# Performance work log

Measured on AMD Instinct MI355X. Metric: run time of the kernel, lower is better.

## Reference

```python
import jax, jax.numpy as jnp
import numpy as np

EPS = 1e-8
HIDDEN = 200


def _dsmall(n, d):
    # torch: d = d*(d>eps) + eps*(d<=eps); n/d
    return n / jnp.where(d > EPS, d, EPS)


def _mp_match(v1, v2, w):
    # v1: (B,S,H); v2: (B,S,H) or (B,H); w: (L,H) -> (B,S,L)
    wt = w.T[None, None]                      # (1,1,H,L)
    a = v1[..., None] * wt                    # (B,S,H,L)
    if v2.ndim == 2:
        v2 = jnp.broadcast_to(v2[:, None, :], v1.shape)
    b = v2[..., None] * wt                    # (B,S,H,L)
    dot = jnp.sum(a * b, axis=2)
    na = jnp.linalg.norm(a, axis=2)
    nb = jnp.linalg.norm(b, axis=2)
    return dot / jnp.maximum(na * nb, EPS)    # cosine_similarity over H


def _mp_pairwise(v1, v2, w):
    # v1: (B,S1,H); v2: (B,S2,H); w: (L,H) -> (B,S1,S2,L)
    a = v1[:, None] * w[None, :, None]        # (B,L,S1,H)
    b = v2[:, None] * w[None, :, None]        # (B,L,S2,H)
    na = jnp.linalg.norm(a, axis=3, keepdims=True)   # (B,L,S1,1)
    nb = jnp.linalg.norm(b, axis=3, keepdims=True)   # (B,L,S2,1)
    n = jnp.einsum('blph,blqh->blpq', a, b)
    d = na * jnp.swapaxes(nb, 2, 3)
    return jnp.transpose(_dsmall(n, d), (0, 2, 3, 1))


def _attention(v1, v2):
    # cosine-similarity matrix (B,S1,S2)
    n1 = jnp.linalg.norm(v1, axis=2, keepdims=True)           # (B,S1,1)
    n2 = jnp.linalg.norm(v2, axis=2, keepdims=True)           # (B,S2,1)
    a = jnp.einsum('bph,bqh->bpq', v1, v2)
    return _dsmall(a, n1 * jnp.swapaxes(n2, 1, 2))


def _matching(con_p, con_h, w1, w2, w3, w4, w5, w6, w7, w8):
    p_fw, p_bw = con_p[..., :HIDDEN], con_p[..., HIDDEN:]
    h_fw, h_bw = con_h[..., :HIDDEN], con_h[..., HIDDEN:]

    # 1) full matching
    mv_p_full_fw = _mp_match(p_fw, h_fw[:, -1, :], w1)
    mv_p_full_bw = _mp_match(p_bw, h_bw[:, 0, :], w2)
    mv_h_full_fw = _mp_match(h_fw, p_fw[:, -1, :], w1)
    mv_h_full_bw = _mp_match(h_bw, p_bw[:, 0, :], w2)

    # 2) maxpooling matching
    mv_max_fw = _mp_pairwise(p_fw, h_fw, w3)  # (B,S1,S2,L)
    mv_max_bw = _mp_pairwise(p_bw, h_bw, w4)
    mv_p_max_fw = jnp.max(mv_max_fw, axis=2)
    mv_p_max_bw = jnp.max(mv_max_bw, axis=2)
    mv_h_max_fw = jnp.max(mv_max_fw, axis=1)
    mv_h_max_bw = jnp.max(mv_max_bw, axis=1)

    # 3) attentive matching (mean)
    att_fw = _attention(p_fw, h_fw)           # (B,S1,S2)
    att_bw = _attention(p_bw, h_bw)

    # sum of att_h over dim 2 is a matmul (same math, no (B,S1,S2,H) tensor)
    att_h_sum_fw = jnp.einsum('bpq,bqh->bph', att_fw, h_fw)
    att_h_sum_bw = jnp.einsum('bpq,bqh->bph', att_bw, h_bw)
    att_p_sum_fw = jnp.einsum('bpq,bph->bqh', att_fw, p_fw)
    att_p_sum_bw = jnp.einsum('bpq,bph->bqh', att_bw, p_bw)

    att_mean_h_fw = _dsmall(att_h_sum_fw, jnp.sum(att_fw, axis=2, keepdims=True))
    att_mean_h_bw = _dsmall(att_h_sum_bw, jnp.sum(att_bw, axis=2, keepdims=True))
    att_mean_p_fw = _dsmall(att_p_sum_fw, jnp.swapaxes(jnp.sum(att_fw, axis=1, keepdims=True), 1, 2))
    att_mean_p_bw = _dsmall(att_p_sum_bw, jnp.swapaxes(jnp.sum(att_bw, axis=1, keepdims=True), 1, 2))

    mv_p_att_mean_fw = _mp_match(p_fw, att_mean_h_fw, w5)
    mv_p_att_mean_bw = _mp_match(p_bw, att_mean_h_bw, w6)
    mv_h_att_mean_fw = _mp_match(h_fw, att_mean_p_fw, w5)
    mv_h_att_mean_bw = _mp_match(h_bw, att_mean_p_bw, w6)

    # 4) max-attentive matching (needs full (B,S1,S2,H) broadcast for the max)
    att_h_fw = h_fw[:, None, :, :] * att_fw[:, :, :, None]   # (B,S1,S2,H)
    att_h_bw = h_bw[:, None, :, :] * att_bw[:, :, :, None]
    att_p_fw = p_fw[:, :, None, :] * att_fw[:, :, :, None]
    att_p_bw = p_bw[:, :, None, :] * att_bw[:, :, :, None]

    att_max_h_fw = jnp.max(att_h_fw, axis=2)                 # (B,S1,H)
    att_max_h_bw = jnp.max(att_h_bw, axis=2)
    att_max_p_fw = jnp.max(att_p_fw, axis=1)                 # (B,S2,H)
    att_max_p_bw = jnp.max(att_p_bw, axis=1)

    mv_p_att_max_fw = _mp_match(p_fw, att_max_h_fw, w7)
    mv_p_att_max_bw = _mp_match(p_bw, att_max_h_bw, w8)
    mv_h_att_max_fw = _mp_match(h_fw, att_max_p_fw, w7)
    mv_h_att_max_bw = _mp_match(h_bw, att_max_p_bw, w8)

    mv_p = jnp.concatenate([mv_p_full_fw, mv_p_max_fw, mv_p_att_mean_fw, mv_p_att_max_fw,
                            mv_p_full_bw, mv_p_max_bw, mv_p_att_mean_bw, mv_p_att_max_bw], axis=2)
    mv_h = jnp.concatenate([mv_h_full_fw, mv_h_max_fw, mv_h_att_mean_fw, mv_h_att_max_fw,
                            mv_h_full_bw, mv_h_max_bw, mv_h_att_mean_bw, mv_h_att_max_bw], axis=2)
    # dropout is identity in inference mode
    return mv_p, mv_h


def setup_inputs() -> dict:
    key = jax.random.key(0)
    ks = jax.random.split(key, 10)
    B, S, H, L = 32, 64, HIDDEN, 20
    w_std = np.sqrt(2.0 / H)  # kaiming_normal fan_in
    inp = {
        'con_p': jax.random.normal(ks[0], (B, S, 2 * H), dtype=jnp.float32),
        'con_h': jax.random.normal(ks[1], (B, S, 2 * H), dtype=jnp.float32),
    }
    for i in range(8):
        inp[f'mp_w{i+1}'] = jax.random.normal(ks[2 + i], (L, H), dtype=jnp.float32) * w_std
    return inp


def reference(con_p, con_h, mp_w1, mp_w2, mp_w3, mp_w4, mp_w5, mp_w6, mp_w7, mp_w8):
    return _matching(con_p, con_h, mp_w1, mp_w2, mp_w3, mp_w4, mp_w5, mp_w6, mp_w7, mp_w8)
```

## Files before the change

kernel.cpp:

```cpp
#include <hip/hip_runtime.h>
#include <hip/hip_bf16.h>
#include <math.h>

#define EPS 1e-8f
#define BB 32
#define SS 64
#define HH 200
#define LL 20
#define KST 232
#define S16ST 72
#define BHST 72
#define MLST 208

typedef short bf16x8 __attribute__((ext_vector_type(8)));
typedef float f32x4 __attribute__((ext_vector_type(4)));
typedef _Float16 f16x8v __attribute__((ext_vector_type(8)));
typedef _Float16 f16x2 __attribute__((ext_vector_type(2)));

__global__ __launch_bounds__(512, 4) void fused_all_kernel(
        const float* __restrict__ conp, const float* __restrict__ conh,
        const float* __restrict__ w1, const float* __restrict__ w2,
        const float* __restrict__ w3, const float* __restrict__ w4,
        const float* __restrict__ w5, const float* __restrict__ w6,
        const float* __restrict__ w7, const float* __restrict__ w8,
        float* __restrict__ out) {
    __shared__ __align__(16) float smem[19104];
    int t = threadIdx.x;

    int wg = ((blockIdx.x & 7) * 96) + (blockIdx.x >> 3);
    int grp = wg / 3;
    int rem = wg % 3;

    if (rem < 2) {
        _Float16* AT16 = (_Float16*)smem;
        _Float16* BT16 = (_Float16*)(smem + 1856);
        _Float16* BHh  = (_Float16*)(smem + 9280);
        _Float16* S16h = (_Float16*)(smem + 16768);
        float* nrmA  = smem + 17344;
        float* nrmB  = smem + 17360;
        _Float16* meanLh = (_Float16*)(smem + 17440);
        _Float16* PB = (_Float16*)smem;
        _Float16* WB = (_Float16*)(smem + 5568);

        int blk = grp * 2 + rem;
        int qh = blk & 3;
        int sdb = blk >> 2;
        int b = sdb & 31, sd = sdb >> 5;
        int dir = sd & 1, side = sd >> 1;
        const float* selfb = side ? conh : conp;
        const float* oppb  = side ? conp : conh;
        int fidx = dir ? 0 : (SS - 1);
        const float* fvr = oppb + (b * SS + fidx) * (2 * HH) + dir * HH;

        int arow = t / 25, ack = t % 25;

        float xr[8], yv0[8];
        if (t < 400) {
            const float* xp = selfb + (b * SS + qh * 16 + arow) * (2 * HH) + dir * HH + ack * 8;
            *(float4*)&xr[0] = *(const float4*)xp; *(float4*)&xr[4] = *(const float4*)(xp + 4);
            *(float4*)&yv0[0] = *(const float4*)(fvr + ack * 8);
            *(float4*)&yv0[4] = *(const float4*)(fvr + ack * 8 + 4);
            f16x8v r8;
#pragma unroll
            for (int i = 0; i < 8; ++i) r8[i] = (_Float16)xr[i];
            *(f16x8v*)&AT16[arow * KST + ack * 8] = r8;
        }
        {
            f16x8v z8 = (f16x8v)(_Float16)0.f;
            if (t < 312) {
                if (t < 48) { int row = t / 3, ckp = 25 + t % 3;
                    *(f16x8v*)&AT16[row * KST + ckp * 8] = z8;
                } else if (t < 240) { int e2 = t - 48; int row = e2 / 3, ckp = 25 + e2 % 3;
                    *(f16x8v*)&BT16[row * KST + ckp * 8] = z8;
                } else { int e2 = t - 240; int row = 200 + e2 / 9, c8 = (e2 % 9) * 8;
                    *(f16x8v*)&BHh[row * BHST + c8] = z8;
                }
            }
        }
        for (int e = t; e < 1600; e += 512) {
            int rw = e / 25, ck = e % 25, k = ck * 8;
            const float* xp = oppb + (b * SS + rw) * (2 * HH) + dir * HH + k;
            float xv[8];
            *(float4*)&xv[0] = *(const float4*)xp; *(float4*)&xv[4] = *(const float4*)(xp + 4);
            f16x8v r8;
#pragma unroll
            for (int i = 0; i < 8; ++i) r8[i] = (_Float16)xv[i];
            *(f16x8v*)&BT16[rw * KST + k] = r8;
        }
        __syncthreads();

        int wv_ = __builtin_amdgcn_readfirstlane(t >> 6);
        int lane = t & 63;
        int q = lane >> 4, c = lane & 15;

        f32x4 accS = (f32x4){0.f, 0.f, 0.f, 0.f};
        if (wv_ < 4) {
            int ct = wv_;
            for (int ks = 0; ks < 7; ++ks) {
                int kb = ks * 32 + q * 8;
                f16x8v af  = *(const f16x8v*)&AT16[c * KST + kb];
                f16x8v bf_ = *(const f16x8v*)&BT16[(ct * 16 + c) * KST + kb];
                accS = __builtin_amdgcn_mfma_f32_16x16x32_f16(af, bf_, accS, 0, 0, 0);
            }
        } else {
            int dt = wv_ - 4;
            f32x4 accB = (f32x4){0.f, 0.f, 0.f, 0.f};
            for (int ks = 0; ks < 7; ++ks) {
                int kb = ks * 32 + q * 8;
                f16x8v bf_ = *(const f16x8v*)&BT16[(dt * 16 + c) * KST + kb];
                accB = __builtin_amdgcn_mfma_f32_16x16x32_f16(bf_, bf_, accB, 0, 0, 0);
            }
            if ((c >> 2) == q) nrmB[dt * 16 + c] = accB[c & 3];
            if (dt == 0) {
                f32x4 accA = (f32x4){0.f, 0.f, 0.f, 0.f};
                for (int ks = 0; ks < 7; ++ks) {
                    int kb = ks * 32 + q * 8;
                    f16x8v af = *(const f16x8v*)&AT16[c * KST + kb];
                    accA = __builtin_amdgcn_mfma_f32_16x16x32_f16(af, af, accA, 0, 0, 0);
                }
                if ((c >> 2) == q) nrmA[c] = accA[c & 3];
            } else {
                for (int ch = dt - 1; ch < 25; ch += 3) {
                    f16x8v v = *(const f16x8v*)&BT16[lane * KST + ch * 8];
#pragma unroll
                    for (int i = 0; i < 8; ++i) BHh[(ch * 8 + i) * BHST + lane] = v[i];
                }
            }
        }
        __syncthreads();

        if (wv_ < 4) {
            int col = wv_ * 16 + c;
            float no = sqrtf(nrmB[col]);
#pragma unroll
            for (int r = 0; r < 4; ++r) {
                int row = q * 4 + r;
                float ns = sqrtf(nrmA[row]);
                S16h[row * S16ST + col] = (_Float16)(accS[r] / fmaxf(ns * no, EPS));
            }
        }
        __syncthreads();

        float wf0[8], wf1[8], wf2[8];
        if (t < 500) {
            int wl = t / 25, wck = t % 25;
            const float* wp0 = (dir ? w2 : w1) + wl * HH + wck * 8;
            const float* wp1 = (dir ? w6 : w5) + wl * HH + wck * 8;
            const float* wp2 = (dir ? w8 : w7) + wl * HH + wck * 8;
            *(float4*)&wf0[0] = *(const float4*)wp0; *(float4*)&wf0[4] = *(const float4*)(wp0 + 4);
            *(float4*)&wf1[0] = *(const float4*)wp1; *(float4*)&wf1[4] = *(const float4*)(wp1 + 4);
            *(float4*)&wf2[0] = *(const float4*)wp2; *(float4*)&wf2[4] = *(const float4*)(wp2 + 4);
        }

        f16x2 mx0, mx1, mx2, mx3;
        {
            f16x2 ninf = {(_Float16)(-INFINITY), (_Float16)(-INFINITY)};
            mx0 = ninf; mx1 = ninf; mx2 = ninf; mx3 = ninf;
        }
        if (wv_ == 7) {
            for (int nt = 0; nt < 13; ++nt) {
                f32x4 macc = (f32x4){0.f, 0.f, 0.f, 0.f};
#pragma unroll
                for (int k2 = 0; k2 < 2; ++k2) {
                    int kb = k2 * 32 + q * 8;
                    f16x8v sa = *(const f16x8v*)&S16h[c * S16ST + kb];
                    f16x8v bh = *(const f16x8v*)&BHh[(nt * 16 + c) * BHST + kb];
                    macc = __builtin_amdgcn_mfma_f32_16x16x32_f16(sa, bh, macc, 0, 0, 0);
                }
                int h = nt * 16 + c;
                if (h < 200) {
#pragma unroll
                    for (int r = 0; r < 4; ++r)
                        meanLh[(q * 4 + r) * MLST + h] = (_Float16)(macc[r] * 0.125f);
                }
            }
        } else if (t < 400) {
            const _Float16* srow = &S16h[arow * S16ST];
            const _Float16* bcol = &BT16[ack * 8];
            for (int kg = 0; kg < 8; ++kg) {
                f16x8v sr = *(const f16x8v*)&srow[kg * 8];
#pragma unroll
                for (int kk = 0; kk < 8; ++kk) {
                    _Float16 sh = sr[kk];
                    f16x2 sv = {sh, sh};
                    f16x8v bv = *(const f16x8v*)&bcol[(kg * 8 + kk) * KST];
                    f16x2 p0 = sv * __builtin_shufflevector(bv, bv, 0, 1);
                    f16x2 p1 = sv * __builtin_shufflevector(bv, bv, 2, 3);
                    f16x2 p2 = sv * __builtin_shufflevector(bv, bv, 4, 5);
                    f16x2 p3 = sv * __builtin_shufflevector(bv, bv, 6, 7);
                    mx0 = __builtin_elementwise_max(mx0, p0);
                    mx1 = __builtin_elementwise_max(mx1, p1);
                    mx2 = __builtin_elementwise_max(mx2, p2);
                    mx3 = __builtin_elementwise_max(mx3, p3);
                }
            }
        }
        __syncthreads();

#pragma unroll
        for (int m = 0; m < 3; ++m) {
            if (t < 400) {
                float yv[8];
                if (m == 0) {
#pragma unroll
                    for (int i = 0; i < 8; ++i) yv[i] = yv0[i];
                } else if (m == 1) {
                    f16x8v yl = *(const f16x8v*)&meanLh[arow * MLST + ack * 8];
#pragma unroll
                    for (int i = 0; i < 8; ++i) yv[i] = (float)yl[i];
                } else {
                    yv[0] = (float)mx0[0]; yv[1] = (float)mx0[1];
                    yv[2] = (float)mx1[0]; yv[3] = (float)mx1[1];
                    yv[4] = (float)mx2[0]; yv[5] = (float)mx2[1];
                    yv[6] = (float)mx3[0]; yv[7] = (float)mx3[1];
                }
                f16x8v r1, r2;
#pragma unroll
                for (int i = 0; i < 8; ++i) {
                    r1[i] = (_Float16)(xr[i] * yv[i]);
                    r2[i] = (_Float16)(yv[i] * yv[i]);
                }
                if (m == 0) {
                    f16x8v r0;
#pragma unroll
                    for (int i = 0; i < 8; ++i) r0[i] = (_Float16)(xr[i] * xr[i]);
                    *(f16x8v*)&PB[(0 * 16 + arow) * KST + ack * 8] = r0;
                }
                *(f16x8v*)&PB[(1 * 16 + arow) * KST + ack * 8] = r1;
                *(f16x8v*)&PB[(2 * 16 + arow) * KST + ack * 8] = r2;
            }
            if (t < 500) {
                int wl = t / 25, wck = t % 25;
                f16x8v wr;
                if (m == 0) {
#pragma unroll
                    for (int i = 0; i < 8; ++i) wr[i] = (_Float16)(wf0[i] * wf0[i]);
                } else if (m == 1) {
#pragma unroll
                    for (int i = 0; i < 8; ++i) wr[i] = (_Float16)(wf1[i] * wf1[i]);
                } else {
#pragma unroll
                    for (int i = 0; i < 8; ++i) wr[i] = (_Float16)(wf2[i] * wf2[i]);
                }
                *(f16x8v*)&WB[wl * KST + wck * 8] = wr;
            }
            if (m == 0) {
                f16x8v z8 = (f16x8v)(_Float16)0.f;
                for (int e = t; e < 540; e += 512) {
                    if (e < 144) { int row = e / 3, ckp = 25 + e % 3;
                        *(f16x8v*)&PB[row * KST + ckp * 8] = z8;
                    } else if (e < 480) { int e2 = e - 144; int row = 20 + e2 / 28, ckp = e2 % 28;
                        *(f16x8v*)&WB[row * KST + ckp * 8] = z8;
                    } else { int e2 = e - 480; int row = e2 / 3, ckp = 25 + e2 % 3;
                        *(f16x8v*)&WB[row * KST + ckp * 8] = z8;
                    }
                }
            }
            __syncthreads();

            if (wv_ < 2) {
                int ntile = wv_;
                f32x4 accA = (f32x4){0.f, 0.f, 0.f, 0.f};
                f32x4 accD = (f32x4){0.f, 0.f, 0.f, 0.f};
                f32x4 accB = (f32x4){0.f, 0.f, 0.f, 0.f};
                for (int ks = 0; ks < 7; ++ks) {
                    int kb = ks * 32 + q * 8;
                    f16x8v bfw = *(const f16x8v*)&WB[(ntile * 16 + c) * KST + kb];
                    f16x8v a0 = *(const f16x8v*)&PB[(0 * 16 + c) * KST + kb];
                    f16x8v a1 = *(const f16x8v*)&PB[(1 * 16 + c) * KST + kb];
                    f16x8v a2 = *(const f16x8v*)&PB[(2 * 16 + c) * KST + kb];
                    accA = __builtin_amdgcn_mfma_f32_16x16x32_f16(a0, bfw, accA, 0, 0, 0);
                    accD = __builtin_amdgcn_mfma_f32_16x16x32_f16(a1, bfw, accD, 0, 0, 0);
                    accB = __builtin_amdgcn_mfma_f32_16x16x32_f16(a2, bfw, accB, 0, 0, 0);
                }
                int l_ = ntile * 16 + c;
                if (l_ < LL) {
                    int chunk = (m == 0) ? 0 : (m == 1) ? 40 : 60;
#pragma unroll
                    for (int r = 0; r < 4; ++r) {
                        int s = qh * 16 + q * 4 + r;
                        float cosv = accD[r] / fmaxf(sqrtf(accA[r] * accB[r]), EPS);
                        out[side * (BB * SS * 160) + (b * SS + s) * 160 + dir * 80 + chunk + l_] = cosv;
                    }
                }
            }
            if (m < 2) __syncthreads();
        }
    } else {
        _Float16* ATr = (_Float16*)smem;
        _Float16* BTr = (_Float16*)(smem + 7424);
        _Float16* w2L = (_Float16*)(smem + 14848);
        float* nA5  = smem + 15432;
        float* nB5  = smem + 15752;
        float* cmL5 = smem + 16072;

        int cblk = grp;
        int lg = cblk & 3;
        int db = cblk >> 2;
        int b = db & 31, dir = db >> 5;
        int l0 = lg * 5;
        const float* wsrc = dir ? w4 : w3;
        const float* Ag = conp + dir * HH;
        const float* Bg = conh + dir * HH;

        for (int e = t; e < 3200; e += 512) {
            int half = (e >= 1600) ? 1 : 0;
            int e2 = e - half * 1600;
            int rw = e2 / 25, ck = e2 % 25, k = ck * 8;
            const float* xp = (half ? Bg : Ag) + (b * SS + rw) * (2 * HH) + k;
            float xv[8];
            *(float4*)&xv[0] = *(const float4*)xp; *(float4*)&xv[4] = *(const float4*)(xp + 4);
            f16x8v r8;
#pragma unroll
            for (int i = 0; i < 8; ++i) r8[i] = (_Float16)xv[i];
            _Float16* dst = half ? BTr : ATr;
            *(f16x8v*)&dst[rw * KST + k] = r8;
        }
        {
            f16x8v z8 = (f16x8v)(_Float16)0.f;
            if (t < 384) {
                int half = (t >= 192) ? 1 : 0;
                int e2 = t - half * 192;
                int row = e2 / 3, ckp = 25 + e2 % 3;
                _Float16* dst = half ? BTr : ATr;
                *(f16x8v*)&dst[row * KST + ckp * 8] = z8;
            } else if (t < 399) {
                int e2 = t - 384;
                int wl = e2 / 3, ckp = 25 + e2 % 3;
                *(f16x8v*)&w2L[wl * KST + ckp * 8] = z8;
            }
            if (t < 125) {
                int wl = t / 25, wck = t % 25;
                const float* wp = wsrc + (l0 + wl) * HH + wck * 8;
                float wvv[8];
                *(float4*)&wvv[0] = *(const float4*)wp; *(float4*)&wvv[4] = *(const float4*)(wp + 4);
                f16x8v r8;
#pragma unroll
                for (int i = 0; i < 8; ++i) r8[i] = (_Float16)(wvv[i] * wvv[i]);
                *(f16x8v*)&w2L[wl * KST + wck * 8] = r8;
            }
        }
        __syncthreads();

        int wv_ = __builtin_amdgcn_readfirstlane(t >> 6);
        int lane = t & 63;
        int q = lane >> 4, c = lane & 15;
        int m0 = (wv_ & 3) * 16;

        f32x4 z4 = (f32x4){0.f, 0.f, 0.f, 0.f};
        f32x4 acc0[4] = {z4, z4, z4, z4};
        f32x4 acc1[4] = {z4, z4, z4, z4};
        f32x4 acc2[4] = {z4, z4, z4, z4};

        if (wv_ < 4) {
            for (int ks = 0; ks < 7; ++ks) {
                int kb = ks * 32 + q * 8;
                f16x8v ar  = *(const f16x8v*)&ATr[(m0 + c) * KST + kb];
                f16x8v ww0 = *(const f16x8v*)&w2L[0 * KST + kb];
                f16x8v ww1 = *(const f16x8v*)&w2L[1 * KST + kb];
                f16x8v ww2 = *(const f16x8v*)&w2L[2 * KST + kb];
                f16x8v af0 = ar * ww0, af1 = ar * ww1, af2 = ar * ww2;
#pragma unroll
                for (int ct = 0; ct < 4; ++ct) {
                    f16x8v br = *(const f16x8v*)&BTr[(ct * 16 + c) * KST + kb];
                    acc0[ct] = __builtin_amdgcn_mfma_f32_16x16x32_f16(af0, br, acc0[ct], 0, 0, 0);
                    acc1[ct] = __builtin_amdgcn_mfma_f32_16x16x32_f16(af1, br, acc1[ct], 0, 0, 0);
                    acc2[ct] = __builtin_amdgcn_mfma_f32_16x16x32_f16(af2, br, acc2[ct], 0, 0, 0);
                }
            }
        } else {
            int d0 = (wv_ - 4) * 16;
            f32x4 nacA[5] = {z4, z4, z4, z4, z4};
            f32x4 nacB[5] = {z4, z4, z4, z4, z4};
            for (int ks = 0; ks < 7; ++ks) {
                int kb = ks * 32 + q * 8;
                f16x8v ar = *(const f16x8v*)&ATr[(d0 + c) * KST + kb];
                f16x8v br = *(const f16x8v*)&BTr[(d0 + c) * KST + kb];
#pragma unroll
                for (int li = 0; li < 5; ++li) {
                    f16x8v wf = *(const f16x8v*)&w2L[li * KST + kb];
                    f16x8v afw = ar * wf;
                    f16x8v bfw = br * wf;
                    nacA[li] = __builtin_amdgcn_mfma_f32_16x16x32_f16(afw, ar, nacA[li], 0, 0, 0);
                    nacB[li] = __builtin_amdgcn_mfma_f32_16x16x32_f16(bfw, br, nacB[li], 0, 0, 0);
                }
            }
            if ((c >> 2) == q) {
#pragma unroll
                for (int li = 0; li < 5; ++li) {
                    nA5[li * 64 + d0 + c] = nacA[li][c & 3];
                    nB5[li * 64 + d0 + c] = nacB[li][c & 3];
                }
            }
        }
        __syncthreads();

#define C_EPI(LI, ACC) do { \
    float na_[4], nb_[4]; \
    _Pragma("unroll") for (int r_ = 0; r_ < 4; ++r_) na_[r_] = sqrtf(nA5[(LI) * 64 + m0 + q * 4 + r_]); \
    _Pragma("unroll") for (int ct_ = 0; ct_ < 4; ++ct_) nb_[ct_] = sqrtf(nB5[(LI) * 64 + ct_ * 16 + c]); \
    float rowm_[4] = {-INFINITY, -INFINITY, -INFINITY, -INFINITY}; \
    float colm_[4] = {-INFINITY, -INFINITY, -INFINITY, -INFINITY}; \
    _Pragma("unroll") for (int ct_ = 0; ct_ < 4; ++ct_) { \
        _Pragma("unroll") for (int r_ = 0; r_ < 4; ++r_) { \
            float cv_ = (ACC)[ct_][r_] / fmaxf(na_[r_] * nb_[ct_], EPS); \
            rowm_[r_] = fmaxf(rowm_[r_], cv_); \
            colm_[ct_] = fmaxf(colm_[ct_], cv_); \
        } \
    } \
    _Pragma("unroll") for (int r_ = 0; r_ < 4; ++r_) { \
        float v_ = rowm_[r_]; \
        v_ = fmaxf(v_, __shfl_xor(v_, 1, 64)); \
        v_ = fmaxf(v_, __shfl_xor(v_, 2, 64)); \
        v_ = fmaxf(v_, __shfl_xor(v_, 4, 64)); \
        v_ = fmaxf(v_, __shfl_xor(v_, 8, 64)); \
        rowm_[r_] = v_; \
    } \
    if (c == 0) { \
        _Pragma("unroll") for (int r_ = 0; r_ < 4; ++r_) \
            out[(b * SS + m0 + q * 4 + r_) * 160 + dir * 80 + 20 + l0 + (LI)] = rowm_[r_]; \
    } \
    _Pragma("unroll") for (int ct_ = 0; ct_ < 4; ++ct_) { \
        float v_ = colm_[ct_]; \
        v_ = fmaxf(v_, __shfl_xor(v_, 16, 64)); \
        v_ = fmaxf(v_, __shfl_xor(v_, 32, 64)); \
        colm_[ct_] = v_; \
    } \
    if (q == 0) { \
        _Pragma("unroll") for (int ct_ = 0; ct_ < 4; ++ct_) \
            cmL5[(LI) * 256 + wv_ * 64 + ct_ * 16 + c] = colm_[ct_]; \
    } \
} while (0)

        if (wv_ < 4) {
            C_EPI(0, acc0);
            C_EPI(1, acc1);
            C_EPI(2, acc2);
            f32x4 acc3[4] = {z4, z4, z4, z4};
            f32x4 acc4[4] = {z4, z4, z4, z4};
            for (int ks = 0; ks < 7; ++ks) {
                int kb = ks * 32 + q * 8;
                f16x8v ar  = *(const f16x8v*)&ATr[(m0 + c) * KST + kb];
                f16x8v ww3 = *(const f16x8v*)&w2L[3 * KST + kb];
                f16x8v ww4 = *(const f16x8v*)&w2L[4 * KST + kb];
                f16x8v af3 = ar * ww3, af4 = ar * ww4;
#pragma unroll
                for (int ct = 0; ct < 4; ++ct) {
                    f16x8v br = *(const f16x8v*)&BTr[(ct * 16 + c) * KST + kb];
                    acc3[ct] = __builtin_amdgcn_mfma_f32_16x16x32_f16(af3, br, acc3[ct], 0, 0, 0);
                    acc4[ct] = __builtin_amdgcn_mfma_f32_16x16x32_f16(af4, br, acc4[ct], 0, 0, 0);
                }
            }
            C_EPI(3, acc3);
            C_EPI(4, acc4);
        }
        __syncthreads();

        if (t < 320) {
            int li = t >> 6, j = t & 63;
            const float* cm = &cmL5[li * 256];
            float mm = fmaxf(fmaxf(cm[j], cm[64 + j]), fmaxf(cm[128 + j], cm[192 + j]));
            out[BB * SS * 160 + (b * SS + j) * 160 + dir * 80 + 20 + l0 + li] = mm;
        }
#undef C_EPI
    }
}

extern "C" void kernel_launch(void* const* d_in, const int* in_sizes, int n_in,
                              void* d_out, int out_size, void* d_ws, size_t ws_size,
                              hipStream_t stream) {
    const float* conp = (const float*)d_in[0];
    const float* conh = (const float*)d_in[1];
    const float* w1 = (const float*)d_in[2];
    const float* w2 = (const float*)d_in[3];
    const float* w3 = (const float*)d_in[4];
    const float* w4 = (const float*)d_in[5];
    const float* w5 = (const float*)d_in[6];
    const float* w6 = (const float*)d_in[7];
    const float* w7 = (const float*)d_in[8];
    const float* w8 = (const float*)d_in[9];
    float* out = (float*)d_out;
    (void)d_ws; (void)ws_size;

    fused_all_kernel<<<768, 512, 0, stream>>>(conp, conh,
                                              w1, w2, w3, w4, w5, w6, w7, w8, out);
}
```

Measured before the change: 101.7 us.

## Process two query tiles per block to reuse loaded opposite-side data

Each matching block now loops over two 16-row query tiles instead of one, so the opposite sequence tile (BT16), its transpose, norms, and weights are loaded and computed once and reused. The grid shrinks from 768 to 512 blocks, with matching and pairwise blocks now interleaved 1:1. Shared-memory layout is rearranged so BT16/BHh persist across the two iterations. This cuts redundant global loads and setup work, but halves the parallelism of the matching path and serialises more work per block.

```diff
diff --git a/kernel.cpp b/kernel.cpp
--- a/kernel.cpp
+++ b/kernel.cpp
@@ -12,7 +12,6 @@
 #define BHST 72
 #define MLST 208
 
-typedef short bf16x8 __attribute__((ext_vector_type(8)));
 typedef float f32x4 __attribute__((ext_vector_type(4)));
 typedef _Float16 f16x8v __attribute__((ext_vector_type(8)));
 typedef _Float16 f16x2 __attribute__((ext_vector_type(2)));
@@ -24,27 +23,30 @@
         const float* __restrict__ w5, const float* __restrict__ w6,
         const float* __restrict__ w7, const float* __restrict__ w8,
         float* __restrict__ out) {
-    __shared__ __align__(16) float smem[19104];
+    __shared__ __align__(16) float smem[19088];
     int t = threadIdx.x;
 
-    int wg = ((blockIdx.x & 7) * 96) + (blockIdx.x >> 3);
-    int grp = wg / 3;
-    int rem = wg % 3;
-
-    if (rem < 2) {
+    int wg = ((blockIdx.x & 7) * 64) + (blockIdx.x >> 3);
+    int grp = wg >> 1;
+    int rem = wg & 1;
+
+    int wv_ = __builtin_amdgcn_readfirstlane(t >> 6);
+    int lane = t & 63;
+    int q = lane >> 4, c = lane & 15;
+
+    if (rem == 0) {
         _Float16* AT16 = (_Float16*)smem;
-        _Float16* BT16 = (_Float16*)(smem + 1856);
-        _Float16* BHh  = (_Float16*)(smem + 9280);
-        _Float16* S16h = (_Float16*)(smem + 16768);
+        _Float16* BHh  = (_Float16*)(smem + 1856);
+        _Float16* S16h = (_Float16*)(smem + 9344);
+        _Float16* BT16 = (_Float16*)(smem + 9920);
         float* nrmA  = smem + 17344;
         float* nrmB  = smem + 17360;
-        _Float16* meanLh = (_Float16*)(smem + 17440);
+        _Float16* meanLh = (_Float16*)(smem + 17424);
         _Float16* PB = (_Float16*)smem;
         _Float16* WB = (_Float16*)(smem + 5568);
 
-        int blk = grp * 2 + rem;
-        int qh = blk & 3;
-        int sdb = blk >> 2;
+        int qp = grp & 1;
+        int sdb = grp >> 1;
         int b = sdb & 31, sd = sdb >> 5;
         int dir = sd & 1, side = sd >> 1;
         const float* selfb = side ? conh : conp;
@@ -54,237 +56,251 @@
 
         int arow = t / 25, ack = t % 25;
 
-        float xr[8], yv0[8];
-        if (t < 400) {
-            const float* xp = selfb + (b * SS + qh * 16 + arow) * (2 * HH) + dir * HH + ack * 8;
-            *(float4*)&xr[0] = *(const float4*)xp; *(float4*)&xr[4] = *(const float4*)(xp + 4);
-            *(float4*)&yv0[0] = *(const float4*)(fvr + ack * 8);
-            *(float4*)&yv0[4] = *(const float4*)(fvr + ack * 8 + 4);
-            f16x8v r8;
-#pragma unroll
-            for (int i = 0; i < 8; ++i) r8[i] = (_Float16)xr[i];
-            *(f16x8v*)&AT16[arow * KST + ack * 8] = r8;
-        }
-        {
-            f16x8v z8 = (f16x8v)(_Float16)0.f;
-            if (t < 312) {
-                if (t < 48) { int row = t / 3, ckp = 25 + t % 3;
+        float yv0[8], wf0[8], wf1[8], wf2[8];
+
+        for (int qi = 0; qi < 2; ++qi) {
+            int qh = qp * 2 + qi;
+            float xr[8];
+
+            if (t < 400) {
+                const float* xp = selfb + (b * SS + qh * 16 + arow) * (2 * HH) + dir * HH + ack * 8;
+                *(float4*)&xr[0] = *(const float4*)xp; *(float4*)&xr[4] = *(const float4*)(xp + 4);
+                if (qi == 0) {
+                    *(float4*)&yv0[0] = *(const float4*)(fvr + ack * 8);
+                    *(float4*)&yv0[4] = *(const float4*)(fvr + ack * 8 + 4);
+                }
+                f16x8v r8;
+#pragma unroll
+                for (int i = 0; i < 8; ++i) r8[i] = (_Float16)xr[i];
+                *(f16x8v*)&AT16[arow * KST + ack * 8] = r8;
+            }
+            {
+                f16x8v z8 = (f16x8v)(_Float16)0.f;
+                if (t < 48) {
+                    int row = t / 3, ckp = 25 + t % 3;
                     *(f16x8v*)&AT16[row * KST + ckp * 8] = z8;
-                } else if (t < 240) { int e2 = t - 48; int row = e2 / 3, ckp = 25 + e2 % 3;
-                    *(f16x8v*)&BT16[row * KST + ckp * 8] = z8;
-                } else { int e2 = t - 240; int row = 200 + e2 / 9, c8 = (e2 % 9) * 8;
-                    *(f16x8v*)&BHh[row * BHST + c8] = z8;
-                }
-            }
-        }
-        for (int e = t; e < 1600; e += 512) {
-            int rw = e / 25, ck = e % 25, k = ck * 8;
-            const float* xp = oppb + (b * SS + rw) * (2 * HH) + dir * HH + k;
-            float xv[8];
-            *(float4*)&xv[0] = *(const float4*)xp; *(float4*)&xv[4] = *(const float4*)(xp + 4);
-            f16x8v r8;
-#pragma unroll
-            for (int i = 0; i < 8; ++i) r8[i] = (_Float16)xv[i];
-            *(f16x8v*)&BT16[rw * KST + k] = r8;
-        }
-        __syncthreads();
-
-        int wv_ = __builtin_amdgcn_readfirstlane(t >> 6);
-        int lane = t & 63;
-        int q = lane >> 4, c = lane & 15;
-
-        f32x4 accS = (f32x4){0.f, 0.f, 0.f, 0.f};
-        if (wv_ < 4) {
-            int ct = wv_;
-            for (int ks = 0; ks < 7; ++ks) {
-                int kb = ks * 32 + q * 8;
-                f16x8v af  = *(const f16x8v*)&AT16[c * KST + kb];
-                f16x8v bf_ = *(const f16x8v*)&BT16[(ct * 16 + c) * KST + kb];
-                accS = __builtin_amdgcn_mfma_f32_16x16x32_f16(af, bf_, accS, 0, 0, 0);
-            }
-        } else {
-            int dt = wv_ - 4;
-            f32x4 accB = (f32x4){0.f, 0.f, 0.f, 0.f};
-            for (int ks = 0; ks < 7; ++ks) {
-                int kb = ks * 32 + q * 8;
-                f16x8v bf_ = *(const f16x8v*)&BT16[(dt * 16 + c) * KST + kb];
-                accB = __builtin_amdgcn_mfma_f32_16x16x32_f16(bf_, bf_, accB, 0, 0, 0);
-            }
-            if ((c >> 2) == q) nrmB[dt * 16 + c] = accB[c & 3];
-            if (dt == 0) {
-                f32x4 accA = (f32x4){0.f, 0.f, 0.f, 0.f};
+                }
+                if (qi == 0) {
+                    if (t >= 48 && t < 240) { int e2 = t - 48; int row = e2 / 3, ckp = 25 + e2 % 3;
+                        *(f16x8v*)&BT16[row * KST + ckp * 8] = z8;
+                    } else if (t >= 240 && t < 312) { int e2 = t - 240; int row = 200 + e2 / 9, c8 = (e2 % 9) * 8;
+                        *(f16x8v*)&BHh[row * BHST + c8] = z8;
+                    }
+                } else {
+                    if (t >= 48 && t < 120) {
+                        int e2 = t - 48; int row = 200 + e2 / 9, c8 = (e2 % 9) * 8;
+                        *(f16x8v*)&BHh[row * BHST + c8] = z8;
+                    }
+                }
+            }
+            if (qi == 0) {
+                for (int e = t; e < 1600; e += 512) {
+                    int rw = e / 25, ck = e % 25, k = ck * 8;
+                    const float* xp = oppb + (b * SS + rw) * (2 * HH) + dir * HH + k;
+                    float xv[8];
+                    *(float4*)&xv[0] = *(const float4*)xp; *(float4*)&xv[4] = *(const float4*)(xp + 4);
+                    f16x8v r8;
+#pragma unroll
+                    for (int i = 0; i < 8; ++i) r8[i] = (_Float16)xv[i];
+                    *(f16x8v*)&BT16[rw * KST + k] = r8;
+                }
+            }
+            __syncthreads();
+
+            f32x4 accS = (f32x4){0.f, 0.f, 0.f, 0.f};
+            if (wv_ < 4) {
+                int ct = wv_;
                 for (int ks = 0; ks < 7; ++ks) {
                     int kb = ks * 32 + q * 8;
-                    f16x8v af = *(const f16x8v*)&AT16[c * KST + kb];
-                    accA = __builtin_amdgcn_mfma_f32_16x16x32_f16(af, af, accA, 0, 0, 0);
-                }
-                if ((c >> 2) == q) nrmA[c] = accA[c & 3];
+                    f16x8v af  = *(const f16x8v*)&AT16[c * KST + kb];
+                    f16x8v bf_ = *(const f16x8v*)&BT16[(ct * 16 + c) * KST + kb];
+                    accS = __builtin_amdgcn_mfma_f32_16x16x32_f16(af, bf_, accS, 0, 0, 0);
+                }
             } else {
-                for (int ch = dt - 1; ch < 25; ch += 3) {
-                    f16x8v v = *(const f16x8v*)&BT16[lane * KST + ch * 8];
-#pragma unroll
-                    for (int i = 0; i < 8; ++i) BHh[(ch * 8 + i) * BHST + lane] = v[i];
-                }
-            }
-        }
-        __syncthreads();
-
-        if (wv_ < 4) {
-            int col = wv_ * 16 + c;
-            float no = sqrtf(nrmB[col]);
-#pragma unroll
-            for (int r = 0; r < 4; ++r) {
-                int row = q * 4 + r;
-                float ns = sqrtf(nrmA[row]);
-                S16h[row * S16ST + col] = (_Float16)(accS[r] / fmaxf(ns * no, EPS));
-            }
-        }
-        __syncthreads();
-
-        float wf0[8], wf1[8], wf2[8];
-        if (t < 500) {
-            int wl = t / 25, wck = t % 25;
-            const float* wp0 = (dir ? w2 : w1) + wl * HH + wck * 8;
-            const float* wp1 = (dir ? w6 : w5) + wl * HH + wck * 8;
-            const float* wp2 = (dir ? w8 : w7) + wl * HH + wck * 8;
-            *(float4*)&wf0[0] = *(const float4*)wp0; *(float4*)&wf0[4] = *(const float4*)(wp0 + 4);
-            *(float4*)&wf1[0] = *(const float4*)wp1; *(float4*)&wf1[4] = *(const float4*)(wp1 + 4);
-            *(float4*)&wf2[0] = *(const float4*)wp2; *(float4*)&wf2[4] = *(const float4*)(wp2 + 4);
-        }
-
-        f16x2 mx0, mx1, mx2, mx3;
-        {
-            f16x2 ninf = {(_Float16)(-INFINITY), (_Float16)(-INFINITY)};
-            mx0 = ninf; mx1 = ninf; mx2 = ninf; mx3 = ninf;
-        }
-        if (wv_ == 7) {
-            for (int nt = 0; nt < 13; ++nt) {
-                f32x4 macc = (f32x4){0.f, 0.f, 0.f, 0.f};
-#pragma unroll
-                for (int k2 = 0; k2 < 2; ++k2) {
-                    int kb = k2 * 32 + q * 8;
-                    f16x8v sa = *(const f16x8v*)&S16h[c * S16ST + kb];
-                    f16x8v bh = *(const f16x8v*)&BHh[(nt * 16 + c) * BHST + kb];
-                    macc = __builtin_amdgcn_mfma_f32_16x16x32_f16(sa, bh, macc, 0, 0, 0);
-                }
-                int h = nt * 16 + c;
-                if (h < 200) {
-#pragma unroll
-                    for (int r = 0; r < 4; ++r)
-                        meanLh[(q * 4 + r) * MLST + h] = (_Float16)(macc[r] * 0.125f);
-                }
-            }
-        } else if (t < 400) {
-            const _Float16* srow = &S16h[arow * S16ST];
-            const _Float16* bcol = &BT16[ack * 8];
-            for (int kg = 0; kg < 8; ++kg) {
-                f16x8v sr = *(const f16x8v*)&srow[kg * 8];
-#pragma unroll
-                for (int kk = 0; kk < 8; ++kk) {
-                    _Float16 sh = sr[kk];
-                    f16x2 sv = {sh, sh};
-                    f16x8v bv = *(const f16x8v*)&bcol[(kg * 8 + kk) * KST];
-                    f16x2 p0 = sv * __builtin_shufflevector(bv, bv, 0, 1);
-                    f16x2 p1 = sv * __builtin_shufflevector(bv, bv, 2, 3);
-                    f16x2 p2 = sv * __builtin_shufflevector(bv, bv, 4, 5);
-                    f16x2 p3 = sv * __builtin_shufflevector(bv, bv, 6, 7);
-                    mx0 = __builtin_elementwise_max(mx0, p0);
-                    mx1 = __builtin_elementwise_max(mx1, p1);
-                    mx2 = __builtin_elementwise_max(mx2, p2);
-                    mx3 = __builtin_elementwise_max(mx3, p3);
-                }
-            }
-        }
-        __syncthreads();
-
-#pragma unroll
-        for (int m = 0; m < 3; ++m) {
-            if (t < 400) {
-                float yv[8];
+                int dt = wv_ - 4;
+                if (qi == 0) {
+                    f32x4 accB = (f32x4){0.f, 0.f, 0.f, 0.f};
+                    for (int ks = 0; ks < 7; ++ks) {
+                        int kb = ks * 32 + q * 8;
+                        f16x8v bf_ = *(const f16x8v*)&BT16[(dt * 16 + c) * KST + kb];
+                        accB = __builtin_amdgcn_mfma_f32_16x16x32_f16(bf_, bf_, accB, 0, 0, 0);
+                    }
+                    if ((c >> 2) == q) nrmB[dt * 16 + c] = accB[c & 3];
+                }
+                if (dt == 0) {
+                    f32x4 accA = (f32x4){0.f, 0.f, 0.f, 0.f};
+                    for (int ks = 0; ks < 7; ++ks) {
+                        int kb = ks * 32 + q * 8;
+                        f16x8v af = *(const f16x8v*)&AT16[c * KST + kb];
+                        accA = __builtin_amdgcn_mfma_f32_16x16x32_f16(af, af, accA, 0, 0, 0);
+                    }
+                    if ((c >> 2) == q) nrmA[c] = accA[c & 3];
+                } else {
+                    for (int ch = dt - 1; ch < 25; ch += 3) {
+                        f16x8v v = *(const f16x8v*)&BT16[lane * KST + ch * 8];
+#pragma unroll
+                        for (int i = 0; i < 8; ++i) BHh[(ch * 8 + i) * BHST + lane] = v[i];
+                    }
+                }
+            }
+            __syncthreads();
+
+            if (wv_ < 4) {
+                int col = wv_ * 16 + c;
+                float no = sqrtf(nrmB[col]);
+#pragma unroll
+                for (int r = 0; r < 4; ++r) {
+                    int row = q * 4 + r;
+                    float ns = sqrtf(nrmA[row]);
+                    S16h[row * S16ST + col] = (_Float16)(accS[r] / fmaxf(ns * no, EPS));
+                }
+            }
+            __syncthreads();
+
+            if (qi == 0 && t < 500) {
+                int wl = t / 25, wck = t % 25;
+                const float* wp0 = (dir ? w2 : w1) + wl * HH + wck * 8;
+                const float* wp1 = (dir ? w6 : w5) + wl * HH + wck * 8;
+                const float* wp2 = (dir ? w8 : w7) + wl * HH + wck * 8;
+                *(float4*)&wf0[0] = *(const float4*)wp0; *(float4*)&wf0[4] = *(const float4*)(wp0 + 4);
+                *(float4*)&wf1[0] = *(const float4*)wp1; *(float4*)&wf1[4] = *(const float4*)(wp1 + 4);
+                *(float4*)&wf2[0] = *(const float4*)wp2; *(float4*)&wf2[4] = *(const float4*)(wp2 + 4);
+            }
+
+            f16x2 mx0, mx1, mx2, mx3;
+            {
+                f16x2 ninf = {(_Float16)(-INFINITY), (_Float16)(-INFINITY)};
+                mx0 = ninf; mx1 = ninf; mx2 = ninf; mx3 = ninf;
+            }
+            if (wv_ == 7) {
+                for (int nt = 0; nt < 13; ++nt) {
+                    f32x4 macc = (f32x4){0.f, 0.f, 0.f, 0.f};
+#pragma unroll
+                    for (int k2 = 0; k2 < 2; ++k2) {
+                        int kb = k2 * 32 + q * 8;
+                        f16x8v sa = *(const f16x8v*)&S16h[c * S16ST + kb];
+                        f16x8v bh = *(const f16x8v*)&BHh[(nt * 16 + c) * BHST + kb];
+                        macc = __builtin_amdgcn_mfma_f32_16x16x32_f16(sa, bh, macc, 0, 0, 0);
+                    }
+                    int h = nt * 16 + c;
+                    if (h < 200) {
+#pragma unroll
+                        for (int r = 0; r < 4; ++r)
+                            meanLh[(q * 4 + r) * MLST + h] = (_Float16)(macc[r] * 0.125f);
+                    }
+                }
+            } else if (t < 400) {
+                const _Float16* srow = &S16h[arow * S16ST];
+                const _Float16* bcol = &BT16[ack * 8];
+                for (int kg = 0; kg < 8; ++kg) {
+                    f16x8v sr = *(const f16x8v*)&srow[kg * 8];
+#pragma unroll
+                    for (int kk = 0; kk < 8; ++kk) {
+                        _Float16 sh = sr[kk];
+                        f16x2 sv = {sh, sh};
+                        f16x8v bv = *(const f16x8v*)&bcol[(kg * 8 + kk) * KST];
+                        f16x2 p0 = sv * __builtin_shufflevector(bv, bv, 0, 1);
+                        f16x2 p1 = sv * __builtin_shufflevector(bv, bv, 2, 3);
+                        f16x2 p2 = sv * __builtin_shufflevector(bv, bv, 4, 5);
+                        f16x2 p3 = sv * __builtin_shufflevector(bv, bv, 6, 7);
+                        mx0 = __builtin_elementwise_max(mx0, p0);
+                        mx1 = __builtin_elementwise_max(mx1, p1);
+                        mx2 = __builtin_elementwise_max(mx2, p2);
+                        mx3 = __builtin_elementwise_max(mx3, p3);
+                    }
+                }
+            }
+            __syncthreads();
+
+#pragma unroll
+            for (int m = 0; m < 3; ++m) {
+                if (t < 400) {
+                    float yv[8];
+                    if (m == 0) {
+#pragma unroll
+                        for (int i = 0; i < 8; ++i) yv[i] = yv0[i];
+                    } else if (m == 1) {
+                        f16x8v yl = *(const f16x8v*)&meanLh[arow * MLST + ack * 8];
+#pragma unroll
+                        for (int i = 0; i < 8; ++i) yv[i] = (float)yl[i];
+                    } else {
+                        yv[0] = (float)mx0[0]; yv[1] = (float)mx0[1];
+                        yv[2] = (float)mx1[0]; yv[3] = (float)mx1[1];
+                        yv[4] = (float)mx2[0]; yv[5] = (float)mx2[1];
+                        yv[6] = (float)mx3[0]; yv[7] = (float)mx3[1];
+                    }
+                    f16x8v r1, r2;
+#pragma unroll
+                    for (int i = 0; i < 8; ++i) {
+                        r1[i] = (_Float16)(xr[i] * yv[i]);
+                        r2[i] = (_Float16)(yv[i] * yv[i]);
+                    }
+                    if (m == 0) {
+                        f16x8v r0;
+#pragma unroll
+                        for (int i = 0; i < 8; ++i) r0[i] = (_Float16)(xr[i] * xr[i]);
+                        *(f16x8v*)&PB[(0 * 16 + arow) * KST + ack * 8] = r0;
+                    }
+                    *(f16x8v*)&PB[(1 * 16 + arow) * KST + ack * 8] = r1;
+                    *(f16x8v*)&PB[(2 * 16 + arow) * KST + ack * 8] = r2;
+                }
+                if (t < 500) {
+                    int wl = t / 25, wck = t % 25;
+                    f16x8v wr;
+                    if (m == 0) {
+#pragma unroll
+                        for (int i = 0; i < 8; ++i) wr[i] = (_Float16)(wf0[i] * wf0[i]);
+                    } else if (m == 1) {
+#pragma unroll
+                        for (int i = 0; i < 8; ++i) wr[i] = (_Float16)(wf1[i] * wf1[i]);
+                    } else {
+#pragma unroll
+                        for (int i = 0; i < 8; ++i) wr[i] = (_Float16)(wf2[i] * wf2[i]);
+                    }
+                    *(f16x8v*)&WB[wl * KST + wck * 8] = wr;
+                }
                 if (m == 0) {
-#pragma unroll
-                    for (int i = 0; i < 8; ++i) yv[i] = yv0[i];
-                } else if (m == 1) {
-                    f16x8v yl = *(const f16x8v*)&meanLh[arow * MLST + ack * 8];
-#pragma unroll
-                    for (int i = 0; i < 8; ++i) yv[i] = (float)yl[i];
-                } else {
-                    yv[0] = (float)mx0[0]; yv[1] = (float)mx0[1];
-                    yv[2] = (float)mx1[0]; yv[3] = (float)mx1[1];
-                    yv[4] = (float)mx2[0]; yv[5] = (float)mx2[1];
-                    yv[6] = (float)mx3[0]; yv[7] = (float)mx3[1];
-                }
-                f16x8v r1, r2;
-#pragma unroll
-                for (int i = 0; i < 8; ++i) {
-                    r1[i] = (_Float16)(xr[i] * yv[i]);
-                    r2[i] = (_Float16)(yv[i] * yv[i]);
-                }
-                if (m == 0) {
-                    f16x8v r0;
-#pragma unroll
-                    for (int i = 0; i < 8; ++i) r0[i] = (_Float16)(xr[i] * xr[i]);
-                    *(f16x8v*)&PB[(0 * 16 + arow) * KST + ack * 8] = r0;
-                }
-                *(f16x8v*)&PB[(1 * 16 + arow) * KST + ack * 8] = r1;
-                *(f16x8v*)&PB[(2 * 16 + arow) * KST + ack * 8] = r2;
-            }
-            if (t < 500) {
-                int wl = t / 25, wck = t % 25;
-                f16x8v wr;
-                if (m == 0) {
-#pragma unroll
-                    for (int i = 0; i < 8; ++i) wr[i] = (_Float16)(wf0[i] * wf0[i]);
-                } else if (m == 1) {
-#pragma unroll
-                    for (int i = 0; i < 8; ++i) wr[i] = (_Float16)(wf1[i] * wf1[i]);
-                } else {
-#pragma unroll
-                    for (int i = 0; i < 8; ++i) wr[i] = (_Float16)(wf2[i] * wf2[i]);
-                }
-                *(f16x8v*)&WB[wl * KST + wck * 8] = wr;
-            }
-            if (m == 0) {
-                f16x8v z8 = (f16x8v)(_Float16)0.f;
-                for (int e = t; e < 540; e += 512) {
-                    if (e < 144) { int row = e / 3, ckp = 25 + e % 3;
-                        *(f16x8v*)&PB[row * KST + ckp * 8] = z8;
-                    } else if (e < 480) { int e2 = e - 144; int row = 20 + e2 / 28, ckp = e2 % 28;
-                        *(f16x8v*)&WB[row * KST + ckp * 8] = z8;
-                    } else { int e2 = e - 480; int row = e2 / 3, ckp = 25 + e2 % 3;
-                        *(f16x8v*)&WB[row * KST + ckp * 8] = z8;
-                    }
-                }
-            }
-            __syncthreads();
-
-            if (wv_ < 2) {
-                int ntile = wv_;
-                f32x4 accA = (f32x4){0.f, 0.f, 0.f, 0.f};
-                f32x4 accD = (f32x4){0.f, 0.f, 0.f, 0.f};
-                f32x4 accB = (f32x4){0.f, 0.f, 0.f, 0.f};
-                for (int ks = 0; ks < 7; ++ks) {
-                    int kb = ks * 32 + q * 8;
-                    f16x8v bfw = *(const f16x8v*)&WB[(ntile * 16 + c) * KST + kb];
-                    f16x8v a0 = *(const f16x8v*)&PB[(0 * 16 + c) * KST + kb];
-                    f16x8v a1 = *(const f16x8v*)&PB[(1 * 16 + c) * KST + kb];
-                    f16x8v a2 = *(const f16x8v*)&PB[(2 * 16 + c) * KST + kb];
-                    accA = __builtin_amdgcn_mfma_f32_16x16x32_f16(a0, bfw, accA, 0, 0, 0);
-                    accD = __builtin_amdgcn_mfma_f32_16x16x32_f16(a1, bfw, accD, 0, 0, 0);
-                    accB = __builtin_amdgcn_mfma_f32_16x16x32_f16(a2, bfw, accB, 0, 0, 0);
-                }
-                int l_ = ntile * 16 + c;
-                if (l_ < LL) {
-                    int chunk = (m == 0) ? 0 : (m == 1) ? 40 : 60;
-#pragma unroll
-                    for (int r = 0; r < 4; ++r) {
-                        int s = qh * 16 + q * 4 + r;
-                        float cosv = accD[r] / fmaxf(sqrtf(accA[r] * accB[r]), EPS);
-                        out[side * (BB * SS * 160) + (b * SS + s) * 160 + dir * 80 + chunk + l_] = cosv;
-                    }
-                }
-            }
-            if (m < 2) __syncthreads();
+                    f16x8v z8 = (f16x8v)(_Float16)0.f;
+                    for (int e = t; e < 540; e += 512) {
+                        if (e < 144) { int row = e / 3, ckp = 25 + e % 3;
+                            *(f16x8v*)&PB[row * KST + ckp * 8] = z8;
+                        } else if (e < 480) { int e2 = e - 144; int row = 20 + e2 / 28, ckp = e2 % 28;
+                            *(f16x8v*)&WB[row * KST + ckp * 8] = z8;
+                        } else { int e2 = e - 480; int row = e2 / 3, ckp = 25 + e2 % 3;
+                            *(f16x8v*)&WB[row * KST + ckp * 8] = z8;
+                        }
+                    }
+                }
+                __syncthreads();
+
+                if (wv_ < 2) {
+                    int ntile = wv_;
+                    f32x4 accA = (f32x4){0.f, 0.f, 0.f, 0.f};
+                    f32x4 accD = (f32x4){0.f, 0.f, 0.f, 0.f};
+                    f32x4 accB = (f32x4){0.f, 0.f, 0.f, 0.f};
+                    for (int ks = 0; ks < 7; ++ks) {
+                        int kb = ks * 32 + q * 8;
+                        f16x8v bfw = *(const f16x8v*)&WB[(ntile * 16 + c) * KST + kb];
+                        f16x8v a0 = *(const f16x8v*)&PB[(0 * 16 + c) * KST + kb];
+                        f16x8v a1 = *(const f16x8v*)&PB[(1 * 16 + c) * KST + kb];
+                        f16x8v a2 = *(const f16x8v*)&PB[(2 * 16 + c) * KST + kb];
+                        accA = __builtin_amdgcn_mfma_f32_16x16x32_f16(a0, bfw, accA, 0, 0, 0);
+                        accD = __builtin_amdgcn_mfma_f32_16x16x32_f16(a1, bfw, accD, 0, 0, 0);
+                        accB = __builtin_amdgcn_mfma_f32_16x16x32_f16(a2, bfw, accB, 0, 0, 0);
+                    }
+                    int l_ = ntile * 16 + c;
+                    if (l_ < LL) {
+                        int chunk = (m == 0) ? 0 : (m == 1) ? 40 : 60;
+#pragma unroll
+                        for (int r = 0; r < 4; ++r) {
+                            int s = qh * 16 + q * 4 + r;
+                            float cosv = accD[r] / fmaxf(sqrtf(accA[r] * accB[r]), EPS);
+                            out[side * (BB * SS * 160) + (b * SS + s) * 160 + dir * 80 + chunk + l_] = cosv;
+                        }
+                    }
+                }
+                if (!(qi == 1 && m == 2)) __syncthreads();
+            }
         }
     } else {
         _Float16* ATr = (_Float16*)smem;
@@ -342,9 +358,6 @@
         }
         __syncthreads();
 
-        int wv_ = __builtin_amdgcn_readfirstlane(t >> 6);
-        int lane = t & 63;
-        int q = lane >> 4, c = lane & 15;
         int m0 = (wv_ & 3) * 16;
 
         f32x4 z4 = (f32x4){0.f, 0.f, 0.f, 0.f};
@@ -482,6 +495,6 @@
     float* out = (float*)d_out;
     (void)d_ws; (void)ws_size;
 
-    fused_all_kernel<<<768, 512, 0, stream>>>(conp, conh,
+    fused_all_kernel<<<512, 512, 0, stream>>>(conp, conh,
                                               w1, w2, w3, w4, w5, w6, w7, w8, out);
 }
```

Result: no change. 102.4 us (+0.6%).
